# Kernel optimization log

Hardware: AMD Instinct MI355X
Metric: run time of the kernel (lower is better)

The kernel has to match this reference:

```python
import jax, jax.numpy as jnp
import numpy as np

EMBED_DIM = 512
NUM_OSC = 64
DT = 0.01
STEPS = 10  # adaptive mode: int(10.0) clamped to [5, 20]


def setup_inputs() -> dict:
    key = jax.random.key(0)
    ks = jax.random.split(key, 12)
    B, S, E, O = 8, 4096, EMBED_DIM, NUM_OSC
    inv = lambda n: 1.0 / np.sqrt(n)
    return {
        "x": jax.random.normal(ks[0], (B, S, E), dtype=jnp.float32),
        "noise": jax.random.normal(ks[1], (B, S, E), dtype=jnp.float32),
        # phase_sync: Linear(E->O), Tanh, Linear(O->O)
        "W1": jax.random.uniform(ks[2], (E, O), jnp.float32, -inv(E), inv(E)),
        "b1": jnp.zeros((O,), jnp.float32),
        "W2": jax.random.uniform(ks[3], (O, O), jnp.float32, -inv(O), inv(O)),
        "b2": jnp.zeros((O,), jnp.float32),
        # fractal_layer: Linear(O->E), ReLU, Linear(E->E)
        "W3": jax.random.uniform(ks[4], (O, E), jnp.float32, -inv(O), inv(O)),
        "b3": jnp.zeros((E,), jnp.float32),
        "W4": jax.random.uniform(ks[5], (E, E), jnp.float32, -inv(E), inv(E)),
        "b4": jnp.zeros((E,), jnp.float32),
        "omega": jax.random.normal(ks[6], (O,), jnp.float32) * 0.1,
        "K": jnp.asarray(1.0, jnp.float32),      # adaptive coupling_strength
        "alpha": jnp.asarray(0.1, jnp.float32),  # adaptive fractal_alpha
    }


def reference(x, noise, W1, b1, W2, b2, W3, b3, W4, b4, omega, K, alpha):
    B, S, E = x.shape
    # phase_sync MLP -> initial phases [B, S, O]
    phases0 = jnp.tanh(x @ W1 + b1) @ W2 + b2

    # Kuramoto evolution: mean-field over oscillator dim each step
    def step(ph, _):
        mean_field = jnp.mean(jnp.sin(ph), axis=-1, keepdims=True)  # [B,S,1]
        dph = omega + K * mean_field * jnp.cos(ph)
        return ph + DT * dph, None

    phases, _ = jax.lax.scan(step, phases0, None, length=STEPS)

    # fractal_layer MLP -> consciousness [B, S, E]
    consciousness = jax.nn.relu(phases @ W3 + b3) @ W4 + b4

    # quaternion assembly: real + 3 copies of modulated noise
    fractal_mod = jnp.sin(alpha * jnp.arange(E, dtype=jnp.float32))  # [E]
    imag = noise[..., None] * fractal_mod[None, None, :, None]       # [B,S,E,1]
    imag = jnp.broadcast_to(imag, (B, S, E, 3))
    return jnp.concatenate([consciousness[..., None], imag], axis=-1)  # [B,S,E,4]
```

## Files before the change

kernel.cpp:

```cpp
#include <hip/hip_runtime.h>
#include <stdint.h>

typedef float f32x4 __attribute__((ext_vector_type(4)));
typedef short bf16x8 __attribute__((ext_vector_type(8)));
typedef uint32_t u32;

#define W1_OFF 0u
#define W2_OFF 16384u
#define W3_OFF 18432u
#define W4_OFF 34816u
#define WS_WEIGHTS_BYTES (165888u * 4u)

__device__ __forceinline__ u32 f2bf(float f) {
  u32 b = __builtin_bit_cast(u32, f);
  return (b + 0x7FFFu + ((b >> 16) & 1u)) >> 16;
}
__device__ __forceinline__ u32 pack2(float lo, float hi) {
  return f2bf(lo) | (f2bf(hi) << 16);
}
__device__ __forceinline__ bf16x8 ld_frag(const u32* p) {
  union { uint4 u; bf16x8 v; } t;
  t.u = *reinterpret_cast<const uint4*>(p);
  return t.v;
}
__device__ __forceinline__ f32x4 mfma16(bf16x8 a, bf16x8 b, f32x4 c) {
  return __builtin_amdgcn_mfma_f32_16x16x32_bf16(a, b, c, 0, 0, 0);
}
__device__ __forceinline__ float fast_tanh(float x) {
  float xc = fminf(15.f, fmaxf(-15.f, x));
  float e = __expf(2.f * xc);
  return 1.f - 2.f * __builtin_amdgcn_rcpf(e + 1.f);
}

__global__ void prep_kernel(const float* __restrict__ W1, const float* __restrict__ W2,
                            const float* __restrict__ W3, const float* __restrict__ W4,
                            u32* __restrict__ ws) {
  int t = blockIdx.x * 256 + threadIdx.x;
  if (t >= 648 * 64) return;
  int f = t >> 6, l = t & 63;
  const float* W; int N, NT, fi; u32 off;
  if (f < 64)       { W = W1; N = 64;  NT = 4;  fi = f;       off = W1_OFF; }
  else if (f < 72)  { W = W2; N = 64;  NT = 4;  fi = f - 64;  off = W2_OFF; }
  else if (f < 136) { W = W3; N = 512; NT = 32; fi = f - 72;  off = W3_OFF; }
  else              { W = W4; N = 512; NT = 32; fi = f - 136; off = W4_OFF; }
  int kt = fi / NT, nt = fi % NT;
  int g = l >> 4, i = l & 15;
  int n = nt * 16 + i;
  int kb = kt * 32 + 4 * g;
  u32 w0 = pack2(W[(size_t)(kb + 0) * N + n],  W[(size_t)(kb + 1) * N + n]);
  u32 w1 = pack2(W[(size_t)(kb + 2) * N + n],  W[(size_t)(kb + 3) * N + n]);
  u32 w2 = pack2(W[(size_t)(kb + 16) * N + n], W[(size_t)(kb + 17) * N + n]);
  u32 w3 = pack2(W[(size_t)(kb + 18) * N + n], W[(size_t)(kb + 19) * N + n]);
  *reinterpret_cast<uint4*>(ws + off + (u32)fi * 256u + (u32)l * 4u) = make_uint4(w0, w1, w2, w3);
}

__global__ __launch_bounds__(512, 4) void mono2_kernel(
    const float* __restrict__ x, const float* __restrict__ noise,
    const u32* __restrict__ ws,
    const float* __restrict__ b1, const float* __restrict__ b2,
    const float* __restrict__ b3, const float* __restrict__ b4,
    const float* __restrict__ omega, const float* __restrict__ Kp,
    const float* __restrict__ alphap, float* __restrict__ out) {
  __shared__ __align__(16) char lds[34816];
  uint4* red = reinterpret_cast<uint4*>(lds);
  uint4* fst = reinterpret_cast<uint4*>(lds);
  uint4* pf  = reinterpret_cast<uint4*>(lds + 32768);
  const int tid = threadIdx.x;
  const int wave = tid >> 6, l = tid & 63;
  const int g = l >> 4, i = l & 15;
  const int tile = blockIdx.x;
  const int m0 = tile * 16;
  const int c0 = wave * 64;

  f32x4 acc1T[4] = {};
#pragma unroll
  for (int kk = 0; kk < 2; ++kk) {
    const int kt = 2 * wave + kk;
    const float* xr = x + (size_t)(m0 + i) * 512 + kt * 32 + 4 * g;
    const float4 a0 = *reinterpret_cast<const float4*>(xr);
    const float4 a1 = *reinterpret_cast<const float4*>(xr + 16);
    union { u32 u[4]; bf16x8 v; } xf;
    xf.u[0] = pack2(a0.x, a0.y); xf.u[1] = pack2(a0.z, a0.w);
    xf.u[2] = pack2(a1.x, a1.y); xf.u[3] = pack2(a1.z, a1.w);
#pragma unroll
    for (int nt = 0; nt < 4; ++nt)
      acc1T[nt] = mfma16(ld_frag(ws + W1_OFF + (u32)(kt * 4 + nt) * 256u + (u32)l * 4u),
                         xf.v, acc1T[nt]);
  }
#pragma unroll
  for (int nt = 0; nt < 4; ++nt)
    red[wave * 256 + nt * 64 + l] = __builtin_bit_cast(uint4, acc1T[nt]);
  __syncthreads();

  if (wave == 0) {
#pragma unroll
    for (int nt = 0; nt < 4; ++nt) {
      f32x4 s = {};
#pragma unroll
      for (int w = 0; w < 8; ++w)
        s += __builtin_bit_cast(f32x4, red[w * 256 + nt * 64 + l]);
      acc1T[nt] = s;
    }
    bf16x8 hfrag[2];
#pragma unroll
    for (int kt2 = 0; kt2 < 2; ++kt2) {
      union { u32 u[4]; bf16x8 v; } t;
#pragma unroll
      for (int q = 0; q < 2; ++q) {
        int nt = 2 * kt2 + q;
        int nb = 16 * nt + 4 * g;
        float v0 = fast_tanh(acc1T[nt][0] + b1[nb + 0]);
        float v1 = fast_tanh(acc1T[nt][1] + b1[nb + 1]);
        float v2 = fast_tanh(acc1T[nt][2] + b1[nb + 2]);
        float v3 = fast_tanh(acc1T[nt][3] + b1[nb + 3]);
        t.u[2 * q + 0] = pack2(v0, v1);
        t.u[2 * q + 1] = pack2(v2, v3);
      }
      hfrag[kt2] = t.v;
    }
    f32x4 acc2T[4] = {};
#pragma unroll
    for (int kt2 = 0; kt2 < 2; ++kt2)
#pragma unroll
      for (int ot = 0; ot < 4; ++ot)
        acc2T[ot] = mfma16(ld_frag(ws + W2_OFF + (u32)(kt2 * 4 + ot) * 256u + (u32)l * 4u),
                           hfrag[kt2], acc2T[ot]);
    float ph[4][4], om[4][4];
    const float Kc = Kp[0];
#pragma unroll
    for (int ot = 0; ot < 4; ++ot) {
      int ob = 16 * ot + 4 * g;
#pragma unroll
      for (int r = 0; r < 4; ++r) {
        ph[ot][r] = acc2T[ot][r] + b2[ob + r];
        om[ot][r] = omega[ob + r];
      }
    }
#pragma unroll
    for (int s = 0; s < 10; ++s) {
      float rs = 0.f;
      float cs[4][4];
#pragma unroll
      for (int ot = 0; ot < 4; ++ot)
#pragma unroll
        for (int r = 0; r < 4; ++r) {
          float sv, cv;
          __sincosf(ph[ot][r], &sv, &cv);
          rs += sv;
          cs[ot][r] = cv;
        }
      rs += __shfl_xor(rs, 16);
      rs += __shfl_xor(rs, 32);
      float sc = 0.01f * Kc * rs * 0.015625f;
#pragma unroll
      for (int ot = 0; ot < 4; ++ot)
#pragma unroll
        for (int r = 0; r < 4; ++r)
          ph[ot][r] += 0.01f * om[ot][r] + sc * cs[ot][r];
    }
#pragma unroll
    for (int kt2 = 0; kt2 < 2; ++kt2) {
      union { u32 u[4]; uint4 u4; } t;
#pragma unroll
      for (int q = 0; q < 2; ++q) {
        int nt = 2 * kt2 + q;
        t.u[2 * q + 0] = pack2(ph[nt][0], ph[nt][1]);
        t.u[2 * q + 1] = pack2(ph[nt][2], ph[nt][3]);
      }
      pf[kt2 * 64 + l] = t.u4;
    }
  }

  const float alpha = alphap[0];
  float nz[16], fmv[4], bbv[4];
#pragma unroll
  for (int nt = 0; nt < 4; ++nt) {
    int col = c0 + nt * 16 + i;
    fmv[nt] = __sinf(alpha * (float)col);
    bbv[nt] = b4[col];
#pragma unroll
    for (int r = 0; r < 4; ++r)
      nz[nt * 4 + r] = noise[(size_t)(m0 + 4 * g + r) * 512 + col];
  }
  __syncthreads();

  {
    bf16x8 pfrag[2];
#pragma unroll
    for (int kt2 = 0; kt2 < 2; ++kt2)
      pfrag[kt2] = __builtin_bit_cast(bf16x8, pf[kt2 * 64 + l]);
    const int c = wave >> 1, qh = wave & 1;
    f32x4 a3[4] = {};
#pragma unroll
    for (int kt2 = 0; kt2 < 2; ++kt2)
#pragma unroll
      for (int nl = 0; nl < 4; ++nl) {
        int nt = 4 * qh + nl;
        a3[nl] = mfma16(ld_frag(ws + W3_OFF + (u32)(kt2 * 32 + c * 8 + nt) * 256u + (u32)l * 4u),
                        pfrag[kt2], a3[nl]);
      }
#pragma unroll
    for (int q = 0; q < 2; ++q) {
      union { u32 u[4]; uint4 u4; } t;
#pragma unroll
      for (int p = 0; p < 2; ++p) {
        int nl = 2 * q + p;
        int nt = 4 * qh + nl;
        int nb = 16 * (8 * c + nt) + 4 * g;
        float v0 = a3[nl][0] + b3[nb + 0]; v0 = v0 > 0.f ? v0 : 0.f;
        float v1 = a3[nl][1] + b3[nb + 1]; v1 = v1 > 0.f ? v1 : 0.f;
        float v2 = a3[nl][2] + b3[nb + 2]; v2 = v2 > 0.f ? v2 : 0.f;
        float v3 = a3[nl][3] + b3[nb + 3]; v3 = v3 > 0.f ? v3 : 0.f;
        t.u[2 * p + 0] = pack2(v0, v1);
        t.u[2 * p + 1] = pack2(v2, v3);
      }
      fst[(4 * c + 2 * qh + q) * 64 + l] = t.u4;
    }
  }
  __syncthreads();

  f32x4 acc[4] = {};
#pragma unroll
  for (int kt = 0; kt < 16; ++kt) {
    union { uint4 u; bf16x8 v; } a;
    a.u = fst[kt * 64 + l];
#pragma unroll
    for (int nt = 0; nt < 4; ++nt)
      acc[nt] = mfma16(a.v,
                       ld_frag(ws + W4_OFF + (u32)(kt * 32 + wave * 4 + nt) * 256u + (u32)l * 4u),
                       acc[nt]);
  }

#pragma unroll
  for (int nt = 0; nt < 4; ++nt) {
    int col = c0 + nt * 16 + i;
#pragma unroll
    for (int r = 0; r < 4; ++r) {
      size_t idx = (size_t)(m0 + 4 * g + r) * 512 + col;
      float im = nz[nt * 4 + r] * fmv[nt];
      float4 o = make_float4(acc[nt][r] + bbv[nt], im, im, im);
      *reinterpret_cast<float4*>(out + idx * 4) = o;
    }
  }
}

extern "C" void kernel_launch(void* const* d_in, const int* in_sizes, int n_in,
                              void* d_out, int out_size, void* d_ws, size_t ws_size,
                              hipStream_t stream) {
  if (ws_size < WS_WEIGHTS_BYTES) return;
  const float* x      = (const float*)d_in[0];
  const float* noise  = (const float*)d_in[1];
  const float* W1     = (const float*)d_in[2];
  const float* b1     = (const float*)d_in[3];
  const float* W2     = (const float*)d_in[4];
  const float* b2     = (const float*)d_in[5];
  const float* W3     = (const float*)d_in[6];
  const float* b3     = (const float*)d_in[7];
  const float* W4     = (const float*)d_in[8];
  const float* b4     = (const float*)d_in[9];
  const float* omega  = (const float*)d_in[10];
  const float* Kp     = (const float*)d_in[11];
  const float* alphap = (const float*)d_in[12];
  u32* ws = (u32*)d_ws;
  prep_kernel<<<162, 256, 0, stream>>>(W1, W2, W3, W4, ws);
  mono2_kernel<<<2048, 512, 0, stream>>>(x, noise, ws, b1, b2, b3, b4,
                                         omega, Kp, alphap, (float*)d_out);
}
```

Before: 127.2 us.

## Process 32-row tiles with 1024-thread blocks to reuse W4 fragments

Each block now handles two 16-row tiles with 16 waves instead of one tile with 8. The waves split the first GEMM across row tiles and K slices, and two waves run the phase evolution in parallel, one per row tile. Each W4 fragment loaded from global memory now feeds MFMAs for both row tiles, halving weight traffic per output row. The noise prefetch before the barrier is dropped, so noise is loaded in the epilogue; with 1024-thread blocks and a larger LDS footprint, register pressure and occupancy may change.

```diff
diff --git a/kernel.cpp b/kernel.cpp
--- a/kernel.cpp
+++ b/kernel.cpp
@@ -54,51 +54,55 @@
   *reinterpret_cast<uint4*>(ws + off + (u32)fi * 256u + (u32)l * 4u) = make_uint4(w0, w1, w2, w3);
 }
 
-__global__ __launch_bounds__(512, 4) void mono2_kernel(
+__global__ __launch_bounds__(1024, 8) void mono3_kernel(
     const float* __restrict__ x, const float* __restrict__ noise,
     const u32* __restrict__ ws,
     const float* __restrict__ b1, const float* __restrict__ b2,
     const float* __restrict__ b3, const float* __restrict__ b4,
     const float* __restrict__ omega, const float* __restrict__ Kp,
     const float* __restrict__ alphap, float* __restrict__ out) {
-  __shared__ __align__(16) char lds[34816];
+  __shared__ __align__(16) char lds[36864];
   uint4* red = reinterpret_cast<uint4*>(lds);
   uint4* fst = reinterpret_cast<uint4*>(lds);
   uint4* pf  = reinterpret_cast<uint4*>(lds + 32768);
   const int tid = threadIdx.x;
   const int wave = tid >> 6, l = tid & 63;
   const int g = l >> 4, i = l & 15;
-  const int tile = blockIdx.x;
-  const int m0 = tile * 16;
-  const int c0 = wave * 64;
-
-  f32x4 acc1T[4] = {};
-#pragma unroll
-  for (int kk = 0; kk < 2; ++kk) {
-    const int kt = 2 * wave + kk;
-    const float* xr = x + (size_t)(m0 + i) * 512 + kt * 32 + 4 * g;
-    const float4 a0 = *reinterpret_cast<const float4*>(xr);
-    const float4 a1 = *reinterpret_cast<const float4*>(xr + 16);
-    union { u32 u[4]; bf16x8 v; } xf;
-    xf.u[0] = pack2(a0.x, a0.y); xf.u[1] = pack2(a0.z, a0.w);
-    xf.u[2] = pack2(a1.x, a1.y); xf.u[3] = pack2(a1.z, a1.w);
+  const int m0 = blockIdx.x * 32;
+  const int c0 = wave * 32;
+
+  if (wave < 8) {
+    const int mt = wave & 1, ks = wave >> 1;
+    f32x4 acc1T[4] = {};
+#pragma unroll
+    for (int kk = 0; kk < 4; ++kk) {
+      const int kt = ks * 4 + kk;
+      const float* xr = x + (size_t)(m0 + mt * 16 + i) * 512 + kt * 32 + 4 * g;
+      const float4 a0 = *reinterpret_cast<const float4*>(xr);
+      const float4 a1 = *reinterpret_cast<const float4*>(xr + 16);
+      union { u32 u[4]; bf16x8 v; } xf;
+      xf.u[0] = pack2(a0.x, a0.y); xf.u[1] = pack2(a0.z, a0.w);
+      xf.u[2] = pack2(a1.x, a1.y); xf.u[3] = pack2(a1.z, a1.w);
+#pragma unroll
+      for (int nt = 0; nt < 4; ++nt)
+        acc1T[nt] = mfma16(ld_frag(ws + W1_OFF + (u32)(kt * 4 + nt) * 256u + (u32)l * 4u),
+                           xf.v, acc1T[nt]);
+    }
 #pragma unroll
     for (int nt = 0; nt < 4; ++nt)
-      acc1T[nt] = mfma16(ld_frag(ws + W1_OFF + (u32)(kt * 4 + nt) * 256u + (u32)l * 4u),
-                         xf.v, acc1T[nt]);
-  }
-#pragma unroll
-  for (int nt = 0; nt < 4; ++nt)
-    red[wave * 256 + nt * 64 + l] = __builtin_bit_cast(uint4, acc1T[nt]);
+      red[((mt * 4 + ks) * 4 + nt) * 64 + l] = __builtin_bit_cast(uint4, acc1T[nt]);
+  }
   __syncthreads();
 
-  if (wave == 0) {
+  if (wave < 2) {
+    const int mt = wave;
+    f32x4 acc1T[4];
 #pragma unroll
     for (int nt = 0; nt < 4; ++nt) {
       f32x4 s = {};
 #pragma unroll
-      for (int w = 0; w < 8; ++w)
-        s += __builtin_bit_cast(f32x4, red[w * 256 + nt * 64 + l]);
+      for (int ks = 0; ks < 4; ++ks)
+        s += __builtin_bit_cast(f32x4, red[((mt * 4 + ks) * 4 + nt) * 64 + l]);
       acc1T[nt] = s;
     }
     bf16x8 hfrag[2];
@@ -167,46 +171,31 @@
         t.u[2 * q + 0] = pack2(ph[nt][0], ph[nt][1]);
         t.u[2 * q + 1] = pack2(ph[nt][2], ph[nt][3]);
       }
-      pf[kt2 * 64 + l] = t.u4;
-    }
-  }
-
-  const float alpha = alphap[0];
-  float nz[16], fmv[4], bbv[4];
-#pragma unroll
-  for (int nt = 0; nt < 4; ++nt) {
-    int col = c0 + nt * 16 + i;
-    fmv[nt] = __sinf(alpha * (float)col);
-    bbv[nt] = b4[col];
-#pragma unroll
-    for (int r = 0; r < 4; ++r)
-      nz[nt * 4 + r] = noise[(size_t)(m0 + 4 * g + r) * 512 + col];
+      pf[mt * 128 + kt2 * 64 + l] = t.u4;
+    }
   }
   __syncthreads();
 
   {
+    const int mt = wave & 1, c = wave >> 1;
     bf16x8 pfrag[2];
 #pragma unroll
     for (int kt2 = 0; kt2 < 2; ++kt2)
-      pfrag[kt2] = __builtin_bit_cast(bf16x8, pf[kt2 * 64 + l]);
-    const int c = wave >> 1, qh = wave & 1;
+      pfrag[kt2] = __builtin_bit_cast(bf16x8, pf[mt * 128 + kt2 * 64 + l]);
     f32x4 a3[4] = {};
 #pragma unroll
     for (int kt2 = 0; kt2 < 2; ++kt2)
 #pragma unroll
-      for (int nl = 0; nl < 4; ++nl) {
-        int nt = 4 * qh + nl;
-        a3[nl] = mfma16(ld_frag(ws + W3_OFF + (u32)(kt2 * 32 + c * 8 + nt) * 256u + (u32)l * 4u),
+      for (int nl = 0; nl < 4; ++nl)
+        a3[nl] = mfma16(ld_frag(ws + W3_OFF + (u32)(kt2 * 32 + c * 4 + nl) * 256u + (u32)l * 4u),
                         pfrag[kt2], a3[nl]);
-      }
 #pragma unroll
     for (int q = 0; q < 2; ++q) {
       union { u32 u[4]; uint4 u4; } t;
 #pragma unroll
       for (int p = 0; p < 2; ++p) {
         int nl = 2 * q + p;
-        int nt = 4 * qh + nl;
-        int nb = 16 * (8 * c + nt) + 4 * g;
+        int nb = 16 * (4 * c + nl) + 4 * g;
         float v0 = a3[nl][0] + b3[nb + 0]; v0 = v0 > 0.f ? v0 : 0.f;
         float v1 = a3[nl][1] + b3[nb + 1]; v1 = v1 > 0.f ? v1 : 0.f;
         float v2 = a3[nl][2] + b3[nb + 2]; v2 = v2 > 0.f ? v2 : 0.f;
@@ -214,32 +203,41 @@
         t.u[2 * p + 0] = pack2(v0, v1);
         t.u[2 * p + 1] = pack2(v2, v3);
       }
-      fst[(4 * c + 2 * qh + q) * 64 + l] = t.u4;
+      fst[mt * 1024 + (2 * c + q) * 64 + l] = t.u4;
     }
   }
   __syncthreads();
 
-  f32x4 acc[4] = {};
+  f32x4 accA[2] = {}, accB[2] = {};
 #pragma unroll
   for (int kt = 0; kt < 16; ++kt) {
-    union { uint4 u; bf16x8 v; } a;
-    a.u = fst[kt * 64 + l];
-#pragma unroll
-    for (int nt = 0; nt < 4; ++nt)
-      acc[nt] = mfma16(a.v,
-                       ld_frag(ws + W4_OFF + (u32)(kt * 32 + wave * 4 + nt) * 256u + (u32)l * 4u),
-                       acc[nt]);
-  }
-
-#pragma unroll
-  for (int nt = 0; nt < 4; ++nt) {
-    int col = c0 + nt * 16 + i;
+    union { uint4 u; bf16x8 v; } aA, aB;
+    aA.u = fst[kt * 64 + l];
+    aB.u = fst[1024 + kt * 64 + l];
+#pragma unroll
+    for (int ntl = 0; ntl < 2; ++ntl) {
+      bf16x8 bf = ld_frag(ws + W4_OFF + (u32)(kt * 32 + wave * 2 + ntl) * 256u + (u32)l * 4u);
+      accA[ntl] = mfma16(aA.v, bf, accA[ntl]);
+      accB[ntl] = mfma16(aB.v, bf, accB[ntl]);
+    }
+  }
+
+  const float alpha = alphap[0];
+#pragma unroll
+  for (int ntl = 0; ntl < 2; ++ntl) {
+    int col = c0 + ntl * 16 + i;
+    float fmv = __sinf(alpha * (float)col);
+    float bbv = b4[col];
 #pragma unroll
     for (int r = 0; r < 4; ++r) {
-      size_t idx = (size_t)(m0 + 4 * g + r) * 512 + col;
-      float im = nz[nt * 4 + r] * fmv[nt];
-      float4 o = make_float4(acc[nt][r] + bbv[nt], im, im, im);
-      *reinterpret_cast<float4*>(out + idx * 4) = o;
+      size_t idxA = (size_t)(m0 + 4 * g + r) * 512 + col;
+      size_t idxB = (size_t)(m0 + 16 + 4 * g + r) * 512 + col;
+      float imA = noise[idxA] * fmv;
+      float imB = noise[idxB] * fmv;
+      float4 oA = make_float4(accA[ntl][r] + bbv, imA, imA, imA);
+      float4 oB = make_float4(accB[ntl][r] + bbv, imB, imB, imB);
+      *reinterpret_cast<float4*>(out + idxA * 4) = oA;
+      *reinterpret_cast<float4*>(out + idxB * 4) = oB;
     }
   }
 }
@@ -263,6 +261,6 @@
   const float* alphap = (const float*)d_in[12];
   u32* ws = (u32*)d_ws;
   prep_kernel<<<162, 256, 0, stream>>>(W1, W2, W3, W4, ws);
-  mono2_kernel<<<2048, 512, 0, stream>>>(x, noise, ws, b1, b2, b3, b4,
-                                         omega, Kp, alphap, (float*)d_out);
-}
+  mono3_kernel<<<1024, 1024, 0, stream>>>(x, noise, ws, b1, b2, b3, b4,
+                                          omega, Kp, alphap, (float*)d_out);
+}
```

Result: faster. 121.4 us (-4.5%).

## Split fused kernel into phase front kernel and MLP back kernel via workspace

Applied to the files above, without the earlier changes.

Splits the monolithic kernel into two launches. The first computes the phase-sync MLP and Kuramoto evolution with 256 threads per block and writes bf16 phase fragments to workspace. The second reads those phases and runs the fractal MLP and quaternion output with a higher occupancy hint. This is meant to stop the serial wave-0 phase section from stalling the other 7 waves and to cut LDS and register pressure, at the cost of an extra launch and a global round trip for the phases.

```diff
diff --git a/kernel.cpp b/kernel.cpp
--- a/kernel.cpp
+++ b/kernel.cpp
@@ -9,7 +9,8 @@
 #define W2_OFF 16384u
 #define W3_OFF 18432u
 #define W4_OFF 34816u
-#define WS_WEIGHTS_BYTES (165888u * 4u)
+#define P_OFF  165888u
+#define WS_NEED_BYTES ((165888ull + 2048ull * 2u * 64u * 4u) * 4ull)
 
 __device__ __forceinline__ u32 f2bf(float f) {
   u32 b = __builtin_bit_cast(u32, f);
@@ -54,51 +55,47 @@
   *reinterpret_cast<uint4*>(ws + off + (u32)fi * 256u + (u32)l * 4u) = make_uint4(w0, w1, w2, w3);
 }
 
-__global__ __launch_bounds__(512, 4) void mono2_kernel(
-    const float* __restrict__ x, const float* __restrict__ noise,
-    const u32* __restrict__ ws,
+__global__ __launch_bounds__(256, 4) void frontP_kernel(
+    const float* __restrict__ x, const u32* __restrict__ wsr, u32* __restrict__ wsw,
     const float* __restrict__ b1, const float* __restrict__ b2,
-    const float* __restrict__ b3, const float* __restrict__ b4,
-    const float* __restrict__ omega, const float* __restrict__ Kp,
-    const float* __restrict__ alphap, float* __restrict__ out) {
-  __shared__ __align__(16) char lds[34816];
-  uint4* red = reinterpret_cast<uint4*>(lds);
-  uint4* fst = reinterpret_cast<uint4*>(lds);
-  uint4* pf  = reinterpret_cast<uint4*>(lds + 32768);
+    const float* __restrict__ omega, const float* __restrict__ Kp) {
+  __shared__ uint4 red[1024];
   const int tid = threadIdx.x;
   const int wave = tid >> 6, l = tid & 63;
   const int g = l >> 4, i = l & 15;
   const int tile = blockIdx.x;
   const int m0 = tile * 16;
-  const int c0 = wave * 64;
-
-  f32x4 acc1T[4] = {};
-#pragma unroll
-  for (int kk = 0; kk < 2; ++kk) {
-    const int kt = 2 * wave + kk;
-    const float* xr = x + (size_t)(m0 + i) * 512 + kt * 32 + 4 * g;
-    const float4 a0 = *reinterpret_cast<const float4*>(xr);
-    const float4 a1 = *reinterpret_cast<const float4*>(xr + 16);
-    union { u32 u[4]; bf16x8 v; } xf;
-    xf.u[0] = pack2(a0.x, a0.y); xf.u[1] = pack2(a0.z, a0.w);
-    xf.u[2] = pack2(a1.x, a1.y); xf.u[3] = pack2(a1.z, a1.w);
+
+  {
+    f32x4 acc1T[4] = {};
+#pragma unroll
+    for (int kk = 0; kk < 4; ++kk) {
+      const int kt = wave * 4 + kk;
+      const float* xr = x + (size_t)(m0 + i) * 512 + kt * 32 + 4 * g;
+      const float4 a0 = *reinterpret_cast<const float4*>(xr);
+      const float4 a1 = *reinterpret_cast<const float4*>(xr + 16);
+      union { u32 u[4]; bf16x8 v; } xf;
+      xf.u[0] = pack2(a0.x, a0.y); xf.u[1] = pack2(a0.z, a0.w);
+      xf.u[2] = pack2(a1.x, a1.y); xf.u[3] = pack2(a1.z, a1.w);
+#pragma unroll
+      for (int nt = 0; nt < 4; ++nt)
+        acc1T[nt] = mfma16(ld_frag(wsr + W1_OFF + (u32)(kt * 4 + nt) * 256u + (u32)l * 4u),
+                           xf.v, acc1T[nt]);
+    }
 #pragma unroll
     for (int nt = 0; nt < 4; ++nt)
-      acc1T[nt] = mfma16(ld_frag(ws + W1_OFF + (u32)(kt * 4 + nt) * 256u + (u32)l * 4u),
-                         xf.v, acc1T[nt]);
-  }
-#pragma unroll
-  for (int nt = 0; nt < 4; ++nt)
-    red[wave * 256 + nt * 64 + l] = __builtin_bit_cast(uint4, acc1T[nt]);
+      red[(wave * 4 + nt) * 64 + l] = __builtin_bit_cast(uint4, acc1T[nt]);
+  }
   __syncthreads();
 
   if (wave == 0) {
+    f32x4 acc1T[4];
 #pragma unroll
     for (int nt = 0; nt < 4; ++nt) {
       f32x4 s = {};
 #pragma unroll
-      for (int w = 0; w < 8; ++w)
-        s += __builtin_bit_cast(f32x4, red[w * 256 + nt * 64 + l]);
+      for (int ks = 0; ks < 4; ++ks)
+        s += __builtin_bit_cast(f32x4, red[(ks * 4 + nt) * 64 + l]);
       acc1T[nt] = s;
     }
     bf16x8 hfrag[2];
@@ -123,7 +120,7 @@
     for (int kt2 = 0; kt2 < 2; ++kt2)
 #pragma unroll
       for (int ot = 0; ot < 4; ++ot)
-        acc2T[ot] = mfma16(ld_frag(ws + W2_OFF + (u32)(kt2 * 4 + ot) * 256u + (u32)l * 4u),
+        acc2T[ot] = mfma16(ld_frag(wsr + W2_OFF + (u32)(kt2 * 4 + ot) * 256u + (u32)l * 4u),
                            hfrag[kt2], acc2T[ot]);
     float ph[4][4], om[4][4];
     const float Kc = Kp[0];
@@ -167,28 +164,35 @@
         t.u[2 * q + 0] = pack2(ph[nt][0], ph[nt][1]);
         t.u[2 * q + 1] = pack2(ph[nt][2], ph[nt][3]);
       }
-      pf[kt2 * 64 + l] = t.u4;
-    }
-  }
-
-  const float alpha = alphap[0];
-  float nz[16], fmv[4], bbv[4];
-#pragma unroll
-  for (int nt = 0; nt < 4; ++nt) {
-    int col = c0 + nt * 16 + i;
-    fmv[nt] = __sinf(alpha * (float)col);
-    bbv[nt] = b4[col];
+      *reinterpret_cast<uint4*>(wsw + P_OFF + ((u32)(tile * 2 + kt2) * 64u + (u32)l) * 4u) = t.u4;
+    }
+  }
+}
+
+__global__ __launch_bounds__(512, 8) void backP_kernel(
+    const float* __restrict__ noise, const u32* __restrict__ ws,
+    const float* __restrict__ b3, const float* __restrict__ b4,
+    const float* __restrict__ alphap, float* __restrict__ out) {
+  __shared__ uint4 fst[1024];
+  const int tid = threadIdx.x;
+  const int wave = tid >> 6, l = tid & 63;
+  const int g = l >> 4, i = l & 15;
+  const int tile = blockIdx.x;
+  const int m0 = tile * 16;
+  const int c0 = wave * 64;
+
+  float nz[16];
+#pragma unroll
+  for (int nt = 0; nt < 4; ++nt)
 #pragma unroll
     for (int r = 0; r < 4; ++r)
-      nz[nt * 4 + r] = noise[(size_t)(m0 + 4 * g + r) * 512 + col];
-  }
-  __syncthreads();
+      nz[nt * 4 + r] = noise[(size_t)(m0 + 4 * g + r) * 512 + c0 + nt * 16 + i];
 
   {
     bf16x8 pfrag[2];
 #pragma unroll
     for (int kt2 = 0; kt2 < 2; ++kt2)
-      pfrag[kt2] = __builtin_bit_cast(bf16x8, pf[kt2 * 64 + l]);
+      pfrag[kt2] = ld_frag(ws + P_OFF + ((u32)(tile * 2 + kt2) * 64u + (u32)l) * 4u);
     const int c = wave >> 1, qh = wave & 1;
     f32x4 a3[4] = {};
 #pragma unroll
@@ -231,14 +235,17 @@
                        acc[nt]);
   }
 
+  const float alpha = alphap[0];
 #pragma unroll
   for (int nt = 0; nt < 4; ++nt) {
     int col = c0 + nt * 16 + i;
+    float fmv = __sinf(alpha * (float)col);
+    float bbv = b4[col];
 #pragma unroll
     for (int r = 0; r < 4; ++r) {
       size_t idx = (size_t)(m0 + 4 * g + r) * 512 + col;
-      float im = nz[nt * 4 + r] * fmv[nt];
-      float4 o = make_float4(acc[nt][r] + bbv[nt], im, im, im);
+      float im = nz[nt * 4 + r] * fmv;
+      float4 o = make_float4(acc[nt][r] + bbv, im, im, im);
       *reinterpret_cast<float4*>(out + idx * 4) = o;
     }
   }
@@ -247,7 +254,7 @@
 extern "C" void kernel_launch(void* const* d_in, const int* in_sizes, int n_in,
                               void* d_out, int out_size, void* d_ws, size_t ws_size,
                               hipStream_t stream) {
-  if (ws_size < WS_WEIGHTS_BYTES) return;
+  if (ws_size < WS_NEED_BYTES) return;
   const float* x      = (const float*)d_in[0];
   const float* noise  = (const float*)d_in[1];
   const float* W1     = (const float*)d_in[2];
@@ -263,6 +270,6 @@
   const float* alphap = (const float*)d_in[12];
   u32* ws = (u32*)d_ws;
   prep_kernel<<<162, 256, 0, stream>>>(W1, W2, W3, W4, ws);
-  mono2_kernel<<<2048, 512, 0, stream>>>(x, noise, ws, b1, b2, b3, b4,
-                                         omega, Kp, alphap, (float*)d_out);
-}
+  frontP_kernel<<<2048, 256, 0, stream>>>(x, ws, ws, b1, b2, omega, Kp);
+  backP_kernel<<<2048, 512, 0, stream>>>(noise, ws, b3, b4, alphap, (float*)d_out);
+}
```

Result: slower. 133.8 us (+5.2%).

## Raise occupancy, rotate serial wave, use nontemporal loads and stores

Applied to the files above, without the earlier changes.

Raises the launch-bounds occupancy target from 4 to 8 blocks per CU, which forces the compiler to use fewer registers. Noise loads now happen after the Kuramoto section and the sin/bias work moves to the epilogue, shortening live ranges. The serial phase/oscillator section is assigned to a different wave per block (blockIdx & 7) to spread the single-wave work across SIMDs. The x loads and output stores use nontemporal hints to cut cache pollution on streaming data. The extra barrier and possible register spills at the tighter bound are the risks.

```diff
diff --git a/kernel.cpp b/kernel.cpp
--- a/kernel.cpp
+++ b/kernel.cpp
@@ -54,7 +54,7 @@
   *reinterpret_cast<uint4*>(ws + off + (u32)fi * 256u + (u32)l * 4u) = make_uint4(w0, w1, w2, w3);
 }
 
-__global__ __launch_bounds__(512, 4) void mono2_kernel(
+__global__ __launch_bounds__(512, 8) void mono8_kernel(
     const float* __restrict__ x, const float* __restrict__ noise,
     const u32* __restrict__ ws,
     const float* __restrict__ b1, const float* __restrict__ b2,
@@ -68,37 +68,40 @@
   const int tid = threadIdx.x;
   const int wave = tid >> 6, l = tid & 63;
   const int g = l >> 4, i = l & 15;
-  const int tile = blockIdx.x;
-  const int m0 = tile * 16;
+  const int m0 = blockIdx.x * 16;
   const int c0 = wave * 64;
-
-  f32x4 acc1T[4] = {};
-#pragma unroll
-  for (int kk = 0; kk < 2; ++kk) {
-    const int kt = 2 * wave + kk;
-    const float* xr = x + (size_t)(m0 + i) * 512 + kt * 32 + 4 * g;
-    const float4 a0 = *reinterpret_cast<const float4*>(xr);
-    const float4 a1 = *reinterpret_cast<const float4*>(xr + 16);
-    union { u32 u[4]; bf16x8 v; } xf;
-    xf.u[0] = pack2(a0.x, a0.y); xf.u[1] = pack2(a0.z, a0.w);
-    xf.u[2] = pack2(a1.x, a1.y); xf.u[3] = pack2(a1.z, a1.w);
+  const int fw = blockIdx.x & 7;
+
+  {
+    f32x4 acc1T[4] = {};
+#pragma unroll
+    for (int kk = 0; kk < 2; ++kk) {
+      const int kt = wave * 2 + kk;
+      const float* xr = x + (size_t)(m0 + i) * 512 + kt * 32 + 4 * g;
+      const f32x4 a0 = __builtin_nontemporal_load(reinterpret_cast<const f32x4*>(xr));
+      const f32x4 a1 = __builtin_nontemporal_load(reinterpret_cast<const f32x4*>(xr + 16));
+      union { u32 u[4]; bf16x8 v; } xf;
+      xf.u[0] = pack2(a0[0], a0[1]); xf.u[1] = pack2(a0[2], a0[3]);
+      xf.u[2] = pack2(a1[0], a1[1]); xf.u[3] = pack2(a1[2], a1[3]);
+#pragma unroll
+      for (int nt = 0; nt < 4; ++nt)
+        acc1T[nt] = mfma16(ld_frag(ws + W1_OFF + (u32)(kt * 4 + nt) * 256u + (u32)l * 4u),
+                           xf.v, acc1T[nt]);
+    }
 #pragma unroll
     for (int nt = 0; nt < 4; ++nt)
-      acc1T[nt] = mfma16(ld_frag(ws + W1_OFF + (u32)(kt * 4 + nt) * 256u + (u32)l * 4u),
-                         xf.v, acc1T[nt]);
-  }
-#pragma unroll
-  for (int nt = 0; nt < 4; ++nt)
-    red[wave * 256 + nt * 64 + l] = __builtin_bit_cast(uint4, acc1T[nt]);
+      red[(wave * 4 + nt) * 64 + l] = __builtin_bit_cast(uint4, acc1T[nt]);
+  }
   __syncthreads();
 
-  if (wave == 0) {
+  if (wave == fw) {
+    f32x4 acc1T[4];
 #pragma unroll
     for (int nt = 0; nt < 4; ++nt) {
       f32x4 s = {};
 #pragma unroll
-      for (int w = 0; w < 8; ++w)
-        s += __builtin_bit_cast(f32x4, red[w * 256 + nt * 64 + l]);
+      for (int ks = 0; ks < 8; ++ks)
+        s += __builtin_bit_cast(f32x4, red[(ks * 4 + nt) * 64 + l]);
       acc1T[nt] = s;
     }
     bf16x8 hfrag[2];
@@ -170,19 +173,14 @@
       pf[kt2 * 64 + l] = t.u4;
     }
   }
-
-  const float alpha = alphap[0];
-  float nz[16], fmv[4], bbv[4];
-#pragma unroll
-  for (int nt = 0; nt < 4; ++nt) {
-    int col = c0 + nt * 16 + i;
-    fmv[nt] = __sinf(alpha * (float)col);
-    bbv[nt] = b4[col];
+  __syncthreads();
+
+  float nz[16];
+#pragma unroll
+  for (int nt = 0; nt < 4; ++nt)
 #pragma unroll
     for (int r = 0; r < 4; ++r)
-      nz[nt * 4 + r] = noise[(size_t)(m0 + 4 * g + r) * 512 + col];
-  }
-  __syncthreads();
+      nz[nt * 4 + r] = noise[(size_t)(m0 + 4 * g + r) * 512 + c0 + nt * 16 + i];
 
   {
     bf16x8 pfrag[2];
@@ -231,15 +229,18 @@
                        acc[nt]);
   }
 
+  const float alpha = alphap[0];
 #pragma unroll
   for (int nt = 0; nt < 4; ++nt) {
     int col = c0 + nt * 16 + i;
+    float fmv = __sinf(alpha * (float)col);
+    float bbv = b4[col];
 #pragma unroll
     for (int r = 0; r < 4; ++r) {
       size_t idx = (size_t)(m0 + 4 * g + r) * 512 + col;
-      float im = nz[nt * 4 + r] * fmv[nt];
-      float4 o = make_float4(acc[nt][r] + bbv[nt], im, im, im);
-      *reinterpret_cast<float4*>(out + idx * 4) = o;
+      float im = nz[nt * 4 + r] * fmv;
+      f32x4 o = {acc[nt][r] + bbv, im, im, im};
+      __builtin_nontemporal_store(o, reinterpret_cast<f32x4*>(out + idx * 4));
     }
   }
 }
@@ -263,6 +264,6 @@
   const float* alphap = (const float*)d_in[12];
   u32* ws = (u32*)d_ws;
   prep_kernel<<<162, 256, 0, stream>>>(W1, W2, W3, W4, ws);
-  mono2_kernel<<<2048, 512, 0, stream>>>(x, noise, ws, b1, b2, b3, b4,
+  mono8_kernel<<<2048, 512, 0, stream>>>(x, noise, ws, b1, b2, b3, b4,
                                          omega, Kp, alphap, (float*)d_out);
 }
```

Result: faster. 112.8 us (-11.3%).
